# Optimization experiments

Hardware: AMD Instinct MI355X
Metric: run time of the kernel (lower is better)

The kernel has to match this reference:

```python
import jax, jax.numpy as jnp
import numpy as np

R, C, B, E, H = 128, 256, 1, 768, 12
DK = E // H


def setup_inputs() -> dict:
    key = jax.random.key(0)
    ks = jax.random.split(key, 6)
    x = jax.random.normal(ks[0], (R, C, B, E), dtype=jnp.float32)
    padding_mask = jnp.zeros((B, R, C), dtype=bool)  # all positions valid
    w_scale = 0.02
    Wq = jax.random.normal(ks[1], (E, E), dtype=jnp.float32) * w_scale
    Wk = jax.random.normal(ks[2], (E, E), dtype=jnp.float32) * w_scale
    Wv = jax.random.normal(ks[3], (E, E), dtype=jnp.float32) * w_scale
    Wo = jax.random.normal(ks[4], (E, E), dtype=jnp.float32) * w_scale
    bq = jnp.zeros((E,), jnp.float32)
    bk = jnp.zeros((E,), jnp.float32)
    bv = jnp.zeros((E,), jnp.float32)
    bo = jnp.zeros((E,), jnp.float32)
    return {"x": x, "padding_mask": padding_mask, "Wq": Wq, "bq": bq,
            "Wk": Wk, "bk": bk, "Wv": Wv, "bv": bv, "Wo": Wo, "bo": bo}


def reference(x, padding_mask, Wq, bq, Wk, bk, Wv, bv, Wo, bo):
    # x: (n_rows=i, n_cols=c, batch=n, embed)
    n_rows, n_cols, batch, embed = x.shape
    d_k = embed // H
    scaling = d_k ** -0.5
    # torch Linear: y = x @ W.T + b
    q = (x @ Wq.T + bq).reshape(n_rows, n_cols, batch, H, d_k) * scaling
    k = (x @ Wk.T + bk).reshape(n_rows, n_cols, batch, H, d_k)
    v = (x @ Wv.T + bv).reshape(n_rows, n_cols, batch, H, d_k)
    # attention over the row axis, independent per column and batch
    attn = jnp.einsum('icnhd,jcnhd->hcnij', q, k)  # (H, C, B, R, R)
    # padding_mask (n, i, c) -> (1, c, n, 1, j), masked keys get -10000
    m = jnp.transpose(padding_mask, (2, 0, 1))[None, :, :, None, :]
    attn = jnp.where(m, jnp.float32(-10000.0), attn)
    probs = jax.nn.softmax(attn, axis=-1)
    # dropout is identity in eval/reference mode
    ctx = jnp.einsum('hcnij,jcnhd->icnhd', probs, v)
    ctx = ctx.reshape(n_rows, n_cols, batch, embed)
    out = ctx @ Wo.T + bo
    return out, probs
```

## Files before the change

### kernel.cpp

```cpp
#include <hip/hip_runtime.h>
#include <hip/hip_bf16.h>

typedef __attribute__((ext_vector_type(8))) short bf16x8;
typedef __attribute__((ext_vector_type(4))) float f32x4;
typedef __attribute__((ext_vector_type(8))) unsigned short u16x8;

#define RR 128
#define CC 256
#define EE 768
#define HH 12
#define DKK 64
#define NQKV 2304

__device__ __forceinline__ unsigned short f2bf(float f) {
  union { float f; unsigned u; } v; v.f = f;
  unsigned u = v.u;
  unsigned r = (u + 0x7fffu + ((u >> 16) & 1u)) >> 16;
  return (unsigned short)r;
}

__device__ __forceinline__ void gload16(const unsigned short* g, char* l) {
  __builtin_amdgcn_global_load_lds((const __attribute__((address_space(1))) void*)g,
                                   (__attribute__((address_space(3))) void*)l, 16, 0, 0);
}

__global__ void cast_all(const float* __restrict__ x, const float* __restrict__ w0,
                         const float* __restrict__ w1, const float* __restrict__ w2,
                         const float* __restrict__ w3, unsigned short* __restrict__ xb,
                         unsigned short* __restrict__ wdst) {
  int b = blockIdx.x;
  const float* src;
  unsigned short* dst;
  int t;
  if (b < 12288) {
    src = x; dst = xb; t = b * 256 + (int)threadIdx.x;
  } else {
    int bb = b - 12288;
    int m = bb / 288;
    src = (m == 0) ? w0 : (m == 1) ? w1 : (m == 2) ? w2 : w3;
    dst = wdst + (size_t)m * 589824;
    t = (bb - m * 288) * 256 + (int)threadIdx.x;
  }
  const float4* s = (const float4*)src + (size_t)t * 2;
  float4 a = s[0], bq = s[1];
  u16x8 o;
  o[0] = f2bf(a.x); o[1] = f2bf(a.y); o[2] = f2bf(a.z); o[3] = f2bf(a.w);
  o[4] = f2bf(bq.x); o[5] = f2bf(bq.y); o[6] = f2bf(bq.z); o[7] = f2bf(bq.w);
  *(u16x8*)(dst + (size_t)t * 8) = o;
}


#define SBAR() do { __builtin_amdgcn_sched_barrier(0); __builtin_amdgcn_s_barrier(); } while (0)
#define SBAR2() do { __builtin_amdgcn_sched_barrier(0); __builtin_amdgcn_s_barrier(); __builtin_amdgcn_sched_barrier(0); } while (0)
#define WAITL() do { asm volatile("s_waitcnt lgkmcnt(0)" ::: "memory"); __builtin_amdgcn_sched_barrier(0); } while (0)
#define WAITV(N) asm volatile("s_waitcnt vmcnt(" #N ")" ::: "memory")

template <int OUTMODE>
__global__ __launch_bounds__(512, 2) void gemm256(
    const unsigned short* __restrict__ A, const unsigned short* __restrict__ Bw,
    void* __restrict__ OutP, const float* __restrict__ bias0,
    const float* __restrict__ bias1, const float* __restrict__ bias2) {
  __shared__ __align__(16) char smem[131072];
  const int nwg = gridDim.x;
  const int chunk = nwg >> 3;
  const int swz = ((int)blockIdx.x & 7) * chunk + ((int)blockIdx.x >> 3);
  const int bm = swz % 128, bn = swz / 128;
  const int r0 = bm << 8, c0 = bn << 8;

  const int tid = threadIdx.x;
  const int w = tid >> 6, lane = tid & 63;
  const int wr = w >> 2, wc = w & 3;
  const int lr = lane & 15, lg = lane >> 4;
  const int l8 = lane >> 3, l7 = lane & 7;
  const int swzc = (l7 ^ (l8 & 7)) << 3;
  const unsigned short* pa = A + (size_t)(r0 + l8) * EE + swzc;
  const unsigned short* pb = Bw + (size_t)(c0 + l8) * EE + swzc;
  const int j0 = w, j1 = w + 8;

  const int aoff = (wr << 14) + (lr << 7);
  const int boff = 32768 + ((wc >> 1) << 14) + ((wc & 1) << 13) + (lr << 7);
  const int sw0 = ((0 + lg) ^ (lr & 7)) << 4;
  const int sw1 = ((4 + lg) ^ (lr & 7)) << 4;

  f32x4 acc[8][4] = {};
  bf16x8 aA[4], aB[4], aC[4], aD[4], bA[4], bB[4];

#define STAGE(s, H, t)                                                        \
  do {                                                                        \
    const unsigned short* _src = ((H) < 2 ? pa : pb) +                        \
        (size_t)(((H) & 1) * 128) * EE + (size_t)(t) * 64;                    \
    char* _d = smem + (s) * 65536 + ((H) >= 2 ? 32768 : 0) + ((H) & 1) * 16384; \
    gload16(_src + (size_t)j0 * 8 * EE, _d + j0 * 1024);                      \
    gload16(_src + (size_t)j1 * 8 * EE, _d + j1 * 1024);                      \
  } while (0)

#define RD_A(dst, g, SW, s)                                                   \
  _Pragma("unroll") for (int _m = 0; _m < 4; ++_m)                            \
      dst[_m] = *(const bf16x8*)(smem + (s) * 65536 + aoff + (g) * 8192 +     \
                                 _m * 2048 + (SW));

#define RD_B(dst, SW, s)                                                      \
  _Pragma("unroll") for (int _n = 0; _n < 4; ++_n)                            \
      dst[_n] = *(const bf16x8*)(smem + (s) * 65536 + boff + _n * 2048 + (SW));

#define MM(g, ar, br)                                                         \
  do {                                                                        \
    __builtin_amdgcn_s_setprio(1);                                            \
    _Pragma("unroll") for (int _i = 0; _i < 4; ++_i)                          \
        _Pragma("unroll") for (int _j = 0; _j < 4; ++_j)                      \
            acc[(g) * 4 + _i][_j] = __builtin_amdgcn_mfma_f32_16x16x32_bf16(  \
                ar[_i], br[_j], acc[(g) * 4 + _i][_j], 0, 0, 0);              \
    __builtin_amdgcn_s_setprio(0);                                            \
  } while (0)

#define ITER(ii, LASTF)                                                        \
  do {                                                                         \
    const int t0 = 2 * (ii), t1 = t0 + 1;                                      \
     RD_A(aA, 0, sw0, 0); RD_B(bA, sw0, 0); STAGE(1, 1, t1);             \
    SBAR(); WAITL(); MM(0, aA, bA); SBAR2();                                   \
     RD_A(aB, 1, sw0, 0); RD_A(aC, 0, sw1, 0); STAGE(1, 2, t1);          \
    SBAR(); WAITL(); MM(1, aB, bA); SBAR2();                                   \
     RD_B(bB, sw1, 0); RD_A(aD, 1, sw1, 0); STAGE(1, 3, t1);             \
    SBAR(); WAITL(); MM(0, aC, bB); SBAR2();                                   \
     if (!(LASTF)) { STAGE(0, 0, t0 + 2); WAITV(2); } else { WAITV(0); } \
    SBAR(); WAITL(); MM(1, aD, bB); SBAR2();                                   \
     RD_A(aA, 0, sw0, 1); RD_B(bA, sw0, 1);                              \
    if (!(LASTF)) STAGE(0, 1, t0 + 2);                                         \
    SBAR(); WAITL(); MM(0, aA, bA); SBAR2();                                   \
     RD_A(aB, 1, sw0, 1); RD_A(aC, 0, sw1, 1);                           \
    if (!(LASTF)) STAGE(0, 2, t0 + 2);                                         \
    SBAR(); WAITL(); MM(1, aB, bA); SBAR2();                                   \
     RD_B(bB, sw1, 1); RD_A(aD, 1, sw1, 1);                              \
    if (!(LASTF)) STAGE(0, 3, t0 + 2);                                         \
    SBAR(); WAITL(); MM(0, aC, bB); SBAR2();                                   \
     if (!(LASTF)) { STAGE(1, 0, t1 + 2); WAITV(2); }                    \
    SBAR(); WAITL(); MM(1, aD, bB); SBAR2();                                   \
  } while (0)

  STAGE(0, 0, 0); STAGE(0, 1, 0); STAGE(0, 2, 0); STAGE(0, 3, 0);
  STAGE(1, 0, 1);
  WAITV(2);
  SBAR2();

#pragma unroll 1
  for (int it = 0; it < 5; ++it) { ITER(it, 0); }
  ITER(5, 1);

#undef STAGE
#undef RD_A
#undef RD_B
#undef MM
#undef ITER

  if constexpr (OUTMODE == 1) {
    unsigned short* sm = (unsigned short*)smem;
    const int mat = bn / 3;
    const float scale = (mat == 0) ? 0.125f : 1.0f;
    const float* bp = (mat == 0) ? bias0 : (mat == 1 ? bias1 : bias2);
    const int cb = c0 - mat * 768;
    float bv4[4];
#pragma unroll
    for (int n = 0; n < 4; ++n) bv4[n] = bp[cb + (wc << 6) + (n << 4) + lr];
#pragma unroll
    for (int m = 0; m < 8; ++m)
#pragma unroll
      for (int n = 0; n < 4; ++n)
#pragma unroll
        for (int r = 0; r < 4; ++r) {
          int row = (wr << 7) + (m << 4) + (lg << 2) + r;
          int col = (wc << 6) + (n << 4) + lr;
          sm[row * 256 + col] = f2bf((acc[m][n][r] + bv4[n]) * scale);
        }
    __syncthreads();
    unsigned short* outm = (unsigned short*)OutP + (size_t)mat * 25165824;
    const int hbase = cb >> 6;
    const int i_idx = r0 >> 8;
#pragma unroll
    for (int p = 0; p < 16; ++p) {
      int idx = p * 512 + tid;
      int row = idx >> 5;
      int hl = (idx >> 3) & 3;
      int d8 = idx & 7;
      *(u16x8*)(outm + ((((size_t)(row * HH + hbase + hl)) << 7 | i_idx) << 6) + d8 * 8) =
          *(const u16x8*)(sm + row * 256 + hl * 64 + d8 * 8);
    }
  } else {
    float* out = (float*)OutP;
    float bv4[4];
#pragma unroll
    for (int n = 0; n < 4; ++n) bv4[n] = bias0[c0 + (wc << 6) + (n << 4) + lr];
#pragma unroll
    for (int m = 0; m < 8; ++m)
#pragma unroll
      for (int n = 0; n < 4; ++n)
#pragma unroll
        for (int r = 0; r < 4; ++r) {
          int u = r0 + (wr << 7) + (m << 4) + (lg << 2) + r;
          int t = ((u & 127) << 8) | (u >> 7);
          int col = (wc << 6) + (n << 4) + lr;
          out[(size_t)t * EE + c0 + col] = acc[m][n][r] + bv4[n];
        }
  }
}

__global__ __launch_bounds__(256, 3) void attn_kernel(
    const unsigned short* __restrict__ qatt, const unsigned short* __restrict__ katt,
    const unsigned short* __restrict__ vatt, const unsigned char* __restrict__ pmask,
    float* __restrict__ probs, unsigned short* __restrict__ ctx) {
  __shared__ unsigned short vt[64 * 136];
  __shared__ unsigned short ps[128 * 136];
  const int bx = blockIdx.x;
  const int c = bx / HH, h = bx - (bx / HH) * HH;
  const int tid = threadIdx.x;
  const int wid = tid >> 6, lane = tid & 63;
  const int lr = lane & 15, lg = lane >> 4;
  const int wr = wid;
  const size_t blk = ((size_t)(c * HH + h)) << 13;
  const unsigned short* qb = qatt + blk;
  const unsigned short* kb = katt + blk;
  const unsigned short* vb = vatt + blk;

  bf16x8 qf[2][2];
#pragma unroll
  for (int m = 0; m < 2; ++m)
#pragma unroll
    for (int kk = 0; kk < 2; ++kk) {
      int qi = (wr << 5) + (m << 4) + lr;
      qf[m][kk] = *(const bf16x8*)(qb + qi * 64 + kk * 32 + (lg << 3));
    }

#pragma unroll
  for (int p = 0; p < 4; ++p) {
    int chunk = p * 256 + tid;
    int j = chunk >> 3, d0 = (chunk & 7) << 3;
    bf16x8 vv = *(const bf16x8*)(vb + j * 64 + d0);
    int jx = j ^ (((d0 >> 3) & 7) << 3);
#pragma unroll
    for (int u = 0; u < 8; ++u) vt[(d0 + u) * 136 + jx] = (unsigned short)vv[u];
  }

  f32x4 s[2][8] = {};
#pragma unroll
  for (int kk = 0; kk < 2; ++kk) {
    bf16x8 kf[8];
#pragma unroll
    for (int n = 0; n < 8; ++n)
      kf[n] = *(const bf16x8*)(kb + (n * 16 + lr) * 64 + kk * 32 + (lg << 3));
#pragma unroll
    for (int m = 0; m < 2; ++m)
#pragma unroll
      for (int n = 0; n < 8; ++n)
        s[m][n] = __builtin_amdgcn_mfma_f32_16x16x32_bf16(qf[m][kk], kf[n],
                                                          s[m][n], 0, 0, 0);
  }

#pragma unroll
  for (int n = 0; n < 8; ++n) {
    if (pmask[(size_t)(n * 16 + lr) * CC + c] != 0) {
      f32x4 neg = {-10000.0f, -10000.0f, -10000.0f, -10000.0f};
      s[0][n] = neg;
      s[1][n] = neg;
    }
  }

  float inv_[2][4];
#pragma unroll
  for (int m = 0; m < 2; ++m) {
    f32x4 mx = s[m][0];
#pragma unroll
    for (int n = 1; n < 8; ++n)
#pragma unroll
      for (int r = 0; r < 4; ++r) mx[r] = fmaxf(mx[r], s[m][n][r]);
#pragma unroll
    for (int r = 0; r < 4; ++r) {
      float t = mx[r];
      t = fmaxf(t, __shfl_xor(t, 1));
      t = fmaxf(t, __shfl_xor(t, 2));
      t = fmaxf(t, __shfl_xor(t, 4));
      t = fmaxf(t, __shfl_xor(t, 8));
      mx[r] = t;
    }
    f32x4 sum = {};
#pragma unroll
    for (int n = 0; n < 8; ++n)
#pragma unroll
      for (int r = 0; r < 4; ++r) {
        float e = exp2f((s[m][n][r] - mx[r]) * 1.44269504f);
        s[m][n][r] = e;
        sum[r] += e;
      }
#pragma unroll
    for (int r = 0; r < 4; ++r) {
      float t = sum[r];
      t += __shfl_xor(t, 1);
      t += __shfl_xor(t, 2);
      t += __shfl_xor(t, 4);
      t += __shfl_xor(t, 8);
      inv_[m][r] = __builtin_amdgcn_rcpf(t);
    }
  }

  const size_t pbase = ((size_t)h * CC + c) * (size_t)(128 * 128);
#pragma unroll
  for (int m = 0; m < 2; ++m)
#pragma unroll
    for (int n = 0; n < 8; ++n)
#pragma unroll
      for (int r = 0; r < 4; ++r) {
        float pv = s[m][n][r] * inv_[m][r];
        int i = (wr << 5) + (m << 4) + (lg << 2) + r;
        int j = (n << 4) + lr;
        probs[pbase + (size_t)i * 128 + j] = pv;
        ps[i * 136 + j] = f2bf(pv);
      }

  __syncthreads();

  f32x4 o[2][4] = {};
#pragma unroll
  for (int kk = 0; kk < 4; ++kk) {
    bf16x8 pa[2], vbr[4];
#pragma unroll
    for (int m = 0; m < 2; ++m)
      pa[m] = *(const bf16x8*)&ps[((wr << 5) + (m << 4) + lr) * 136 + kk * 32 + (lg << 3)];
#pragma unroll
    for (int n = 0; n < 4; ++n) {
      int d = (n << 4) + lr;
      int jb = (kk * 32 + (lg << 3)) ^ ((((d >> 3) & 7)) << 3);
      vbr[n] = *(const bf16x8*)&vt[d * 136 + jb];
    }
#pragma unroll
    for (int m = 0; m < 2; ++m)
#pragma unroll
      for (int n = 0; n < 4; ++n)
        o[m][n] = __builtin_amdgcn_mfma_f32_16x16x32_bf16(pa[m], vbr[n], o[m][n], 0, 0, 0);
  }

  unsigned short* band = ps + wr * 32 * 136;
#pragma unroll
  for (int m = 0; m < 2; ++m)
#pragma unroll
    for (int n = 0; n < 4; ++n)
#pragma unroll
      for (int r = 0; r < 4; ++r) {
        int il = (m << 4) + (lg << 2) + r;
        int d = (n << 4) + lr;
        band[il * 64 + d] = f2bf(o[m][n][r]);
      }
  __syncthreads();

#pragma unroll
  for (int p = 0; p < 4; ++p) {
    int chunk = p * 256 + tid;
    int i = chunk >> 3, d8 = chunk & 7;
    *(u16x8*)(ctx + ((size_t)c * 128 + i) * EE + h * 64 + d8 * 8) =
        *(const u16x8*)(ps + (i >> 5) * (32 * 136) + (i & 31) * 64 + d8 * 8);
  }
}

extern "C" void kernel_launch(void* const* d_in, const int* in_sizes, int n_in,
                              void* d_out, int out_size, void* d_ws, size_t ws_size,
                              hipStream_t stream) {
  const float* x = (const float*)d_in[0];
  const unsigned char* pm = (const unsigned char*)d_in[1];
  const float* Wq = (const float*)d_in[2];
  const float* bq = (const float*)d_in[3];
  const float* Wk = (const float*)d_in[4];
  const float* bk = (const float*)d_in[5];
  const float* Wv = (const float*)d_in[6];
  const float* bv = (const float*)d_in[7];
  const float* Wo = (const float*)d_in[8];
  const float* bo = (const float*)d_in[9];

  unsigned short* ws = (unsigned short*)d_ws;
  unsigned short* xb = ws;
  unsigned short* qkv = xb + 25165824;
  unsigned short* wcast = qkv + 75497472;

  float* outp = (float*)d_out;
  float* probs = outp + 25165824;

  cast_all<<<13440, 256, 0, stream>>>(x, Wq, Wk, Wv, Wo, xb, wcast);
  gemm256<1><<<1152, 512, 0, stream>>>(xb, wcast, (void*)qkv, bq, bk, bv);
  attn_kernel<<<CC * HH, 256, 0, stream>>>(qkv, qkv + 25165824, qkv + 50331648,
                                           pm, probs, xb );
  gemm256<0><<<384, 512, 0, stream>>>(xb, wcast + 1769472, (void*)outp, bo,
                                      nullptr, nullptr);
}
```

Before: 345.8 us.

## Restructure attention to one block per column looping heads with double-buffered K/V prefetch

```diff
diff --git a/kernel.cpp b/kernel.cpp
--- a/kernel.cpp
+++ b/kernel.cpp
@@ -203,92 +203,114 @@
   }
 }
 
-__global__ __launch_bounds__(256, 3) void attn_kernel(
+__global__ __launch_bounds__(512, 2) void attn_col(
     const unsigned short* __restrict__ qatt, const unsigned short* __restrict__ katt,
     const unsigned short* __restrict__ vatt, const unsigned char* __restrict__ pmask,
     float* __restrict__ probs, unsigned short* __restrict__ ctx) {
-  __shared__ unsigned short vt[64 * 136];
-  __shared__ unsigned short ps[128 * 136];
-  const int bx = blockIdx.x;
-  const int c = bx / HH, h = bx - (bx / HH) * HH;
+  __shared__ unsigned short sm[53248];
+  const int c = blockIdx.x;
   const int tid = threadIdx.x;
-  const int wid = tid >> 6, lane = tid & 63;
+  const int w = tid >> 6, lane = tid & 63;
   const int lr = lane & 15, lg = lane >> 4;
-  const int wr = wid;
-  const size_t blk = ((size_t)(c * HH + h)) << 13;
-  const unsigned short* qb = qatt + blk;
-  const unsigned short* kb = katt + blk;
-  const unsigned short* vb = vatt + blk;
-
-  bf16x8 qf[2][2];
-#pragma unroll
-  for (int m = 0; m < 2; ++m)
+  const int j0 = tid >> 3;
+  const int j1 = 64 + j0;
+  const int d00 = (tid & 7) << 3;
+  const int kst0 = j0 * 72 + d00, kst1 = j1 * 72 + d00;
+  unsigned short* ps = sm + 35840;
+  const size_t cb12 = (size_t)c * HH;
+
+  unsigned char pmv[8];
+#pragma unroll
+  for (int n = 0; n < 8; ++n) pmv[n] = pmask[(size_t)((n << 4) + lr) * CC + c];
+
+  {
+    const unsigned short* kb = katt + (cb12 << 13);
+    const unsigned short* vb = vatt + (cb12 << 13);
+    bf16x8 k0 = *(const bf16x8*)(kb + j0 * 64 + d00);
+    bf16x8 k1 = *(const bf16x8*)(kb + j1 * 64 + d00);
+    bf16x8 v0 = *(const bf16x8*)(vb + j0 * 64 + d00);
+    bf16x8 v1 = *(const bf16x8*)(vb + j1 * 64 + d00);
+    *(bf16x8*)(sm + kst0) = k0;
+    *(bf16x8*)(sm + kst1) = k1;
+    unsigned short* vt0 = sm + 18432;
+#pragma unroll
+    for (int u = 0; u < 8; ++u) vt0[(d00 + u) * 136 + j0] = (unsigned short)v0[u];
+#pragma unroll
+    for (int u = 0; u < 8; ++u) vt0[(d00 + u) * 136 + j1] = (unsigned short)v1[u];
+  }
+  bf16x8 qf0, qf1;
+  {
+    const unsigned short* qb = qatt + (cb12 << 13);
+    qf0 = *(const bf16x8*)(qb + ((w << 4) + lr) * 64 + (lg << 3));
+    qf1 = *(const bf16x8*)(qb + ((w << 4) + lr) * 64 + 32 + (lg << 3));
+  }
+  __syncthreads();
+
+  int cur = 0;
+#pragma unroll 1
+  for (int h = 0; h < HH; ++h) {
+    const unsigned short* ksc = sm + cur * 9216;
+    const unsigned short* vtc = sm + 18432 + cur * 8704;
+
+    bf16x8 kr0{}, kr1{}, vr0{}, vr1{}, qn0{}, qn1{};
+    const bool pf = (h + 1 < HH);
+    if (pf) {
+      const unsigned short* kb = katt + ((cb12 + h + 1) << 13);
+      const unsigned short* vb = vatt + ((cb12 + h + 1) << 13);
+      const unsigned short* qb = qatt + ((cb12 + h + 1) << 13);
+      kr0 = *(const bf16x8*)(kb + j0 * 64 + d00);
+      kr1 = *(const bf16x8*)(kb + j1 * 64 + d00);
+      vr0 = *(const bf16x8*)(vb + j0 * 64 + d00);
+      vr1 = *(const bf16x8*)(vb + j1 * 64 + d00);
+      qn0 = *(const bf16x8*)(qb + ((w << 4) + lr) * 64 + (lg << 3));
+      qn1 = *(const bf16x8*)(qb + ((w << 4) + lr) * 64 + 32 + (lg << 3));
+    }
+
+    f32x4 s[8] = {};
 #pragma unroll
     for (int kk = 0; kk < 2; ++kk) {
-      int qi = (wr << 5) + (m << 4) + lr;
-      qf[m][kk] = *(const bf16x8*)(qb + qi * 64 + kk * 32 + (lg << 3));
-    }
-
-#pragma unroll
-  for (int p = 0; p < 4; ++p) {
-    int chunk = p * 256 + tid;
-    int j = chunk >> 3, d0 = (chunk & 7) << 3;
-    bf16x8 vv = *(const bf16x8*)(vb + j * 64 + d0);
-    int jx = j ^ (((d0 >> 3) & 7) << 3);
-#pragma unroll
-    for (int u = 0; u < 8; ++u) vt[(d0 + u) * 136 + jx] = (unsigned short)vv[u];
-  }
-
-  f32x4 s[2][8] = {};
-#pragma unroll
-  for (int kk = 0; kk < 2; ++kk) {
-    bf16x8 kf[8];
-#pragma unroll
-    for (int n = 0; n < 8; ++n)
-      kf[n] = *(const bf16x8*)(kb + (n * 16 + lr) * 64 + kk * 32 + (lg << 3));
-#pragma unroll
-    for (int m = 0; m < 2; ++m)
+      bf16x8 kf[8];
 #pragma unroll
       for (int n = 0; n < 8; ++n)
-        s[m][n] = __builtin_amdgcn_mfma_f32_16x16x32_bf16(qf[m][kk], kf[n],
-                                                          s[m][n], 0, 0, 0);
-  }
-
-#pragma unroll
-  for (int n = 0; n < 8; ++n) {
-    if (pmask[(size_t)(n * 16 + lr) * CC + c] != 0) {
-      f32x4 neg = {-10000.0f, -10000.0f, -10000.0f, -10000.0f};
-      s[0][n] = neg;
-      s[1][n] = neg;
-    }
-  }
-
-  float inv_[2][4];
-#pragma unroll
-  for (int m = 0; m < 2; ++m) {
-    f32x4 mx = s[m][0];
+        kf[n] = *(const bf16x8*)&ksc[((n << 4) + lr) * 72 + kk * 32 + (lg << 3)];
+      bf16x8 q = kk ? qf1 : qf0;
+#pragma unroll
+      for (int n = 0; n < 8; ++n)
+        s[n] = __builtin_amdgcn_mfma_f32_16x16x32_bf16(q, kf[n], s[n], 0, 0, 0);
+    }
+
+#pragma unroll
+    for (int n = 0; n < 8; ++n) {
+      if (pmv[n]) {
+        f32x4 neg = {-10000.0f, -10000.0f, -10000.0f, -10000.0f};
+        s[n] = neg;
+      }
+    }
+
+    f32x4 mxv = s[0];
 #pragma unroll
     for (int n = 1; n < 8; ++n)
 #pragma unroll
-      for (int r = 0; r < 4; ++r) mx[r] = fmaxf(mx[r], s[m][n][r]);
+      for (int r = 0; r < 4; ++r) mxv[r] = fmaxf(mxv[r], s[n][r]);
 #pragma unroll
     for (int r = 0; r < 4; ++r) {
-      float t = mx[r];
+      float t = mxv[r];
       t = fmaxf(t, __shfl_xor(t, 1));
       t = fmaxf(t, __shfl_xor(t, 2));
       t = fmaxf(t, __shfl_xor(t, 4));
       t = fmaxf(t, __shfl_xor(t, 8));
-      mx[r] = t;
+      mxv[r] = t;
     }
     f32x4 sum = {};
 #pragma unroll
     for (int n = 0; n < 8; ++n)
 #pragma unroll
       for (int r = 0; r < 4; ++r) {
-        float e = exp2f((s[m][n][r] - mx[r]) * 1.44269504f);
-        s[m][n][r] = e;
+        float e = exp2f((s[n][r] - mxv[r]) * 1.44269504f);
+        s[n][r] = e;
         sum[r] += e;
       }
+    float inv_[4];
 #pragma unroll
     for (int r = 0; r < 4; ++r) {
       float t = sum[r];
@@ -296,65 +318,62 @@
       t += __shfl_xor(t, 2);
       t += __shfl_xor(t, 4);
       t += __shfl_xor(t, 8);
-      inv_[m][r] = __builtin_amdgcn_rcpf(t);
-    }
-  }
-
-  const size_t pbase = ((size_t)h * CC + c) * (size_t)(128 * 128);
-#pragma unroll
-  for (int m = 0; m < 2; ++m)
+      inv_[r] = __builtin_amdgcn_rcpf(t);
+    }
+
+    const size_t pbase = ((size_t)h * CC + c) << 14;
 #pragma unroll
     for (int n = 0; n < 8; ++n)
 #pragma unroll
       for (int r = 0; r < 4; ++r) {
-        float pv = s[m][n][r] * inv_[m][r];
-        int i = (wr << 5) + (m << 4) + (lg << 2) + r;
+        float pv = s[n][r] * inv_[r];
+        int i = (w << 4) + (lg << 2) + r;
         int j = (n << 4) + lr;
         probs[pbase + (size_t)i * 128 + j] = pv;
         ps[i * 136 + j] = f2bf(pv);
       }
 
-  __syncthreads();
-
-  f32x4 o[2][4] = {};
-#pragma unroll
-  for (int kk = 0; kk < 4; ++kk) {
-    bf16x8 pa[2], vbr[4];
-#pragma unroll
-    for (int m = 0; m < 2; ++m)
-      pa[m] = *(const bf16x8*)&ps[((wr << 5) + (m << 4) + lr) * 136 + kk * 32 + (lg << 3)];
-#pragma unroll
-    for (int n = 0; n < 4; ++n) {
-      int d = (n << 4) + lr;
-      int jb = (kk * 32 + (lg << 3)) ^ ((((d >> 3) & 7)) << 3);
-      vbr[n] = *(const bf16x8*)&vt[d * 136 + jb];
-    }
-#pragma unroll
-    for (int m = 0; m < 2; ++m)
+    f32x4 o[4] = {};
+#pragma unroll
+    for (int kk = 0; kk < 4; ++kk) {
+      bf16x8 pa = *(const bf16x8*)&ps[((w << 4) + lr) * 136 + kk * 32 + (lg << 3)];
+      bf16x8 vbr[4];
 #pragma unroll
       for (int n = 0; n < 4; ++n)
-        o[m][n] = __builtin_amdgcn_mfma_f32_16x16x32_bf16(pa[m], vbr[n], o[m][n], 0, 0, 0);
-  }
-
-  unsigned short* band = ps + wr * 32 * 136;
-#pragma unroll
-  for (int m = 0; m < 2; ++m)
+        vbr[n] = *(const bf16x8*)&vtc[((n << 4) + lr) * 136 + kk * 32 + (lg << 3)];
+#pragma unroll
+      for (int n = 0; n < 4; ++n)
+        o[n] = __builtin_amdgcn_mfma_f32_16x16x32_bf16(pa, vbr[n], o[n], 0, 0, 0);
+    }
+
+    if (pf) {
+      unsigned short* ksn = sm + (cur ^ 1) * 9216;
+      unsigned short* vtn = sm + 18432 + (cur ^ 1) * 8704;
+      *(bf16x8*)(ksn + kst0) = kr0;
+      *(bf16x8*)(ksn + kst1) = kr1;
+#pragma unroll
+      for (int u = 0; u < 8; ++u) vtn[(d00 + u) * 136 + j0] = (unsigned short)vr0[u];
+#pragma unroll
+      for (int u = 0; u < 8; ++u) vtn[(d00 + u) * 136 + j1] = (unsigned short)vr1[u];
+      qf0 = qn0; qf1 = qn1;
+    }
+
+    unsigned short* bandc = ps + ((w << 4) * 136);
 #pragma unroll
     for (int n = 0; n < 4; ++n)
 #pragma unroll
-      for (int r = 0; r < 4; ++r) {
-        int il = (m << 4) + (lg << 2) + r;
-        int d = (n << 4) + lr;
-        band[il * 64 + d] = f2bf(o[m][n][r]);
-      }
-  __syncthreads();
-
-#pragma unroll
-  for (int p = 0; p < 4; ++p) {
-    int chunk = p * 256 + tid;
-    int i = chunk >> 3, d8 = chunk & 7;
-    *(u16x8*)(ctx + ((size_t)c * 128 + i) * EE + h * 64 + d8 * 8) =
-        *(const u16x8*)(ps + (i >> 5) * (32 * 136) + (i & 31) * 64 + d8 * 8);
+      for (int r = 0; r < 4; ++r)
+        bandc[((lg << 2) + r) * 64 + (n << 4) + lr] = f2bf(o[n][r]);
+#pragma unroll
+    for (int q = 0; q < 2; ++q) {
+      int fl = q * 64 + lane;
+      int iL = fl >> 3, d8 = fl & 7;
+      *(u16x8*)(ctx + ((size_t)c * 128 + (w << 4) + iL) * EE + h * 64 + d8 * 8) =
+          *(const u16x8*)(bandc + iL * 64 + d8 * 8);
+    }
+
+    __syncthreads();
+    cur ^= 1;
   }
 }
 
@@ -382,8 +401,8 @@
 
   cast_all<<<13440, 256, 0, stream>>>(x, Wq, Wk, Wv, Wo, xb, wcast);
   gemm256<1><<<1152, 512, 0, stream>>>(xb, wcast, (void*)qkv, bq, bk, bv);
-  attn_kernel<<<CC * HH, 256, 0, stream>>>(qkv, qkv + 25165824, qkv + 50331648,
-                                           pm, probs, xb );
+  attn_col<<<CC, 512, 0, stream>>>(qkv, qkv + 25165824, qkv + 50331648,
+                                   pm, probs, xb );
   gemm256<0><<<384, 512, 0, stream>>>(xb, wcast + 1769472, (void*)outp, bo,
                                       nullptr, nullptr);
 }
```

New measurement: 326.6 us. 5.6% less time.
